# Performance work log

Measured on AMD Instinct MI355X. Metric: run time of the kernel, lower is better.

The kernel has to match this reference:

```python
import jax, jax.numpy as jnp
import numpy as np

H = 2048      # hidden_dim
NH = 32       # num_heads
HD = H // NH  # head_dim


def setup_inputs() -> dict:
    key = jax.random.key(0)
    ks = jax.random.split(key, 9)
    s = 1.0 / np.sqrt(H)
    return {
        "hidden_states": jax.random.normal(ks[0], (2, 2048, H), dtype=jnp.float32),
        "wq": jax.random.uniform(ks[1], (H, H), jnp.float32, -s, s),
        "bq": jnp.zeros((H,), jnp.float32),
        "wk": jax.random.uniform(ks[2], (H, H), jnp.float32, -s, s),
        "bk": jnp.zeros((H,), jnp.float32),
        "wv": jax.random.uniform(ks[3], (H, H), jnp.float32, -s, s),
        "bv": jnp.zeros((H,), jnp.float32),
        "wo": jax.random.uniform(ks[4], (H, H), jnp.float32, -s, s),
        "bo": jnp.zeros((H,), jnp.float32),
    }


def reference(hidden_states, wq, bq, wk, bk, wv, bv, wo, bo):
    B, S, _ = hidden_states.shape
    def heads(x):  # [B,S,H] -> [B,NH,S,HD]
        return x.reshape(B, S, NH, HD).transpose(0, 2, 1, 3)
    q = heads(hidden_states @ wq.T + bq)
    k = heads(hidden_states @ wk.T + bk)
    v = heads(hidden_states @ wv.T + bv)
    scores = jnp.einsum("bhqd,bhkd->bhqk", q, k) / np.sqrt(HD).astype(np.float32)
    causal = jnp.tril(jnp.ones((S, S), dtype=bool))
    scores = jnp.where(causal, scores, -jnp.inf)
    attn = jax.nn.softmax(scores, axis=-1)
    out = jnp.einsum("bhqk,bhkd->bhqd", attn, v)
    out = out.transpose(0, 2, 1, 3).reshape(B, S, H)
    return out @ wo.T + bo
```

## Files before the change

### kernel.cpp

```cpp
#include <hip/hip_runtime.h>
#include <hip/hip_bf16.h>

#define HDIM 2048
#define NHEADS 32
#define HEADD 64
#define NBATCH 2
#define SEQLEN 2048
#define MTOT (NBATCH * SEQLEN)
#define NQT (SEQLEN / 128)
#define LDQKV 6144

typedef __bf16 bf16;
typedef __bf16 bf16x8 __attribute__((ext_vector_type(8)));
typedef float f32x4 __attribute__((ext_vector_type(4)));
typedef float f32x8 __attribute__((ext_vector_type(8)));
typedef float f32x16 __attribute__((ext_vector_type(16)));

__device__ __forceinline__ void gload_lds16(const bf16* g, bf16* l) {
  __builtin_amdgcn_global_load_lds(
      (const __attribute__((address_space(1))) void*)g,
      (__attribute__((address_space(3))) void*)l, 16, 0, 0);
}

__device__ __forceinline__ unsigned cvtpk_bf16(float lo, float hi) {
  unsigned r;
  asm("v_cvt_pk_bf16_f32 %0, %1, %2" : "=v"(r) : "v"(lo), "v"(hi));
  return r;
}

__device__ __forceinline__ float max3f(float a, float b, float c) {
  float r;
  asm("v_max3_f32 %0, %1, %2, %3" : "=v"(r) : "v"(a), "v"(b), "v"(c));
  return r;
}

__global__ void __launch_bounds__(256) cvt_f32_to_bf16(
    const float* __restrict__ src, bf16* __restrict__ dst, int n) {
  int i = (blockIdx.x * 256 + threadIdx.x) * 8;
  if (i >= n) return;
  f32x8 a = *(const f32x8*)(src + i);
  bf16x8 o;
#pragma unroll
  for (int j = 0; j < 8; ++j) o[j] = (bf16)a[j];
  *(bf16x8*)(dst + i) = o;
}

__global__ void __launch_bounds__(256) cvt4_f32_to_bf16(
    const float* __restrict__ s0, const float* __restrict__ s1,
    const float* __restrict__ s2, const float* __restrict__ s3,
    bf16* __restrict__ d0, bf16* __restrict__ d1,
    bf16* __restrict__ d2, bf16* __restrict__ d3) {
  const float* src; bf16* dst;
  switch (blockIdx.y) {
    case 0: src = s0; dst = d0; break;
    case 1: src = s1; dst = d1; break;
    case 2: src = s2; dst = d2; break;
    default: src = s3; dst = d3; break;
  }
  int i = (blockIdx.x * 256 + threadIdx.x) * 8;
  f32x8 a = *(const f32x8*)(src + i);
  bf16x8 o;
#pragma unroll
  for (int j = 0; j < 8; ++j) o[j] = (bf16)a[j];
  *(bf16x8*)(dst + i) = o;
}

__global__ void __launch_bounds__(256) pack_bias(
    const float* __restrict__ bq, const float* __restrict__ bk,
    const float* __restrict__ bv, float* __restrict__ out) {
  int i = blockIdx.x * 256 + threadIdx.x;
  if (i >= LDQKV) return;
  float v;
  if (i < HDIM) v = bq[i];
  else if (i < 2 * HDIM) v = bk[i - HDIM];
  else v = bv[i - 2 * HDIM];
  out[i] = v;
}

template <bool OUT_F32>
__global__ void __launch_bounds__(256, 2) gemmq(
    const bf16* __restrict__ A, const bf16* __restrict__ W,
    const float* __restrict__ bias, void* __restrict__ Cout,
    int Ndim, float scale) {
  constexpr int NT = 64;
  __shared__ bf16 As[2][256 * 32];
  __shared__ bf16 Bs[3][192 * 32];

  const int tid = threadIdx.x;
  const int l = tid & 63;
  const int w = tid >> 6;
  const int wm = w >> 1;
  const int wn = w & 1;

  const int wid = blockIdx.x;
  const int j = wid >> 3;
  const int m0 = ((wid & 7) * 2 + (j & 1)) * 256;
  const int n0 = (j >> 1) * 192;

  const int rowA = tid >> 2;
  const int cg = (((tid & 3) ^ ((tid >> 3) & 3))) * 8;

  auto stgA = [&](int s, int kt) {
    const bf16* g = A + (size_t)m0 * 2048 + kt * 32 + cg;
#pragma unroll
    for (int i = 0; i < 4; ++i)
      gload_lds16(g + (size_t)(i * 64 + rowA) * 2048,
                  &As[s][(i * 256 + w * 64) * 8]);
  };
  auto stgB = [&](int s, int kt) {
    const bf16* g = W + (size_t)n0 * 2048 + kt * 32 + cg;
#pragma unroll
    for (int i = 0; i < 3; ++i)
      gload_lds16(g + (size_t)(i * 64 + rowA) * 2048,
                  &Bs[s][(i * 256 + w * 64) * 8]);
  };

  f32x4 acc[8][6];
#pragma unroll
  for (int mf = 0; mf < 8; ++mf)
#pragma unroll
    for (int nf = 0; nf < 6; ++nf) acc[mf][nf] = {0.f, 0.f, 0.f, 0.f};

  const int fr = l & 15;
  const int fch = (((l >> 4) ^ ((fr >> 1) & 3))) * 8;
  const int abase = (wm * 128 + fr) * 32 + fch;
  const int bbase = (wn * 96 + fr) * 32 + fch;

  stgA(0, 0);
  stgB(0, 0);
  stgB(1, 1);
  asm volatile("s_waitcnt vmcnt(3)" ::: "memory");
  __builtin_amdgcn_s_barrier();

  int sb = 0;
  for (int t = 0; t < NT; ++t) {
    const int sa = t & 1;
    int sb2 = sb + 2; if (sb2 >= 3) sb2 -= 3;

    bf16x8 bf[6], af[4];
#pragma unroll
    for (int nf = 0; nf < 6; ++nf)
      bf[nf] = *(const bf16x8*)&Bs[sb][bbase + nf * 16 * 32];
#pragma unroll
    for (int f = 0; f < 4; ++f)
      af[f] = *(const bf16x8*)&As[sa][abase + f * 16 * 32];

    if (t + 1 < NT) stgA(sa ^ 1, t + 1);
    if (t + 2 < NT) stgB(sb2, t + 2);

    __builtin_amdgcn_s_setprio(1);
#pragma unroll
    for (int f = 0; f < 4; ++f)
#pragma unroll
      for (int nf = 0; nf < 6; ++nf)
        acc[f][nf] = __builtin_amdgcn_mfma_f32_16x16x32_bf16(
            af[f], bf[nf], acc[f][nf], 0, 0, 0);
    __builtin_amdgcn_s_setprio(0);

#pragma unroll
    for (int f = 0; f < 4; ++f)
      af[f] = *(const bf16x8*)&As[sa][abase + (4 + f) * 16 * 32];

    __builtin_amdgcn_s_setprio(1);
#pragma unroll
    for (int f = 0; f < 4; ++f)
#pragma unroll
      for (int nf = 0; nf < 6; ++nf)
        acc[4 + f][nf] = __builtin_amdgcn_mfma_f32_16x16x32_bf16(
            af[f], bf[nf], acc[4 + f][nf], 0, 0, 0);
    __builtin_amdgcn_s_setprio(0);

    if (t < NT - 2)
      asm volatile("s_waitcnt vmcnt(3)" ::: "memory");
    else
      asm volatile("s_waitcnt vmcnt(0)" ::: "memory");
    __builtin_amdgcn_s_barrier();

    sb = (sb == 2) ? 0 : sb + 1;
  }

  const int rj = (l >> 4) * 4;
#pragma unroll
  for (int mf = 0; mf < 8; ++mf)
#pragma unroll
    for (int nf = 0; nf < 6; ++nf) {
      const int col = n0 + wn * 96 + nf * 16 + fr;
      const float secsc = (col < 2048) ? scale : 1.0f;
      const float bvl = bias[col];
#pragma unroll
      for (int jj = 0; jj < 4; ++jj) {
        const int row = m0 + wm * 128 + mf * 16 + rj + jj;
        const float v = (acc[mf][nf][jj] + bvl) * secsc;
        if constexpr (OUT_F32)
          ((float*)Cout)[(size_t)row * Ndim + col] = v;
        else
          ((bf16*)Cout)[(size_t)row * Ndim + col] = (bf16)v;
      }
    }
}

__global__ void __launch_bounds__(256, 2) gemmp(
    const bf16* __restrict__ A, const bf16* __restrict__ W,
    const float* __restrict__ bias, float* __restrict__ Cout,
    int Ndim) {
  constexpr int NT = 64;
  __shared__ bf16 As[2][128 * 32];
  __shared__ bf16 Bs[3][128 * 32];

  const int tid = threadIdx.x;
  const int l = tid & 63;
  const int w = tid >> 6;
  const int wm = w >> 1;
  const int wn = w & 1;

  const int wid = blockIdx.x;
  const int j = wid >> 3;
  const int m0 = ((wid & 7) * 4 + (j & 3)) * 128;
  const int n0 = (j >> 2) * 128;

  const int rowA = tid >> 2;
  const int cg = (((tid & 3) ^ ((tid >> 3) & 3))) * 8;

  auto stgA = [&](int s, int kt) {
    const bf16* g = A + (size_t)m0 * 2048 + kt * 32 + cg;
#pragma unroll
    for (int i = 0; i < 2; ++i)
      gload_lds16(g + (size_t)(i * 64 + rowA) * 2048,
                  &As[s][(i * 256 + w * 64) * 8]);
  };
  auto stgB = [&](int s, int kt) {
    const bf16* g = W + (size_t)n0 * 2048 + kt * 32 + cg;
#pragma unroll
    for (int i = 0; i < 2; ++i)
      gload_lds16(g + (size_t)(i * 64 + rowA) * 2048,
                  &Bs[s][(i * 256 + w * 64) * 8]);
  };

  f32x4 acc[4][4];
#pragma unroll
  for (int mf = 0; mf < 4; ++mf)
#pragma unroll
    for (int nf = 0; nf < 4; ++nf) acc[mf][nf] = {0.f, 0.f, 0.f, 0.f};

  const int fr = l & 15;
  const int fch = (((l >> 4) ^ ((fr >> 1) & 3))) * 8;
  const int abase = (wm * 64 + fr) * 32 + fch;
  const int bbase = (wn * 64 + fr) * 32 + fch;

  stgA(0, 0);
  stgB(0, 0);
  stgB(1, 1);
  asm volatile("s_waitcnt vmcnt(2)" ::: "memory");
  __builtin_amdgcn_s_barrier();

  int sb = 0;
  for (int t = 0; t < NT; ++t) {
    const int sa = t & 1;
    int sb2 = sb + 2; if (sb2 >= 3) sb2 -= 3;

    bf16x8 bf[4], af[4];
#pragma unroll
    for (int nf = 0; nf < 4; ++nf)
      bf[nf] = *(const bf16x8*)&Bs[sb][bbase + nf * 16 * 32];
#pragma unroll
    for (int f = 0; f < 4; ++f)
      af[f] = *(const bf16x8*)&As[sa][abase + f * 16 * 32];

    if (t + 1 < NT) stgA(sa ^ 1, t + 1);
    if (t + 2 < NT) stgB(sb2, t + 2);

    __builtin_amdgcn_s_setprio(1);
#pragma unroll
    for (int f = 0; f < 4; ++f)
#pragma unroll
      for (int nf = 0; nf < 4; ++nf)
        acc[f][nf] = __builtin_amdgcn_mfma_f32_16x16x32_bf16(
            af[f], bf[nf], acc[f][nf], 0, 0, 0);
    __builtin_amdgcn_s_setprio(0);

    if (t < NT - 2)
      asm volatile("s_waitcnt vmcnt(2)" ::: "memory");
    else
      asm volatile("s_waitcnt vmcnt(0)" ::: "memory");
    __builtin_amdgcn_s_barrier();

    sb = (sb == 2) ? 0 : sb + 1;
  }

  const int rj = (l >> 4) * 4;
#pragma unroll
  for (int mf = 0; mf < 4; ++mf)
#pragma unroll
    for (int nf = 0; nf < 4; ++nf) {
      const int col = n0 + wn * 64 + nf * 16 + fr;
      const float bvl = bias[col];
#pragma unroll
      for (int jj = 0; jj < 4; ++jj) {
        const int row = m0 + wm * 64 + mf * 16 + rj + jj;
        Cout[(size_t)row * Ndim + col] = acc[mf][nf][jj] + bvl;
      }
    }
}

__global__ void __launch_bounds__(256) transpose_v(
    const bf16* __restrict__ QKV, bf16* __restrict__ Vt) {
  __shared__ bf16 T[64][72];
  const int t = threadIdx.x;
  const int s0 = blockIdx.x * 64;
  const int h = blockIdx.y, b = blockIdx.z;
  const size_t inb = (size_t)b * SEQLEN * LDQKV + 2 * HDIM + (size_t)h * HEADD;
#pragma unroll
  for (int i = 0; i < 2; ++i) {
    const int idx = t + i * 256;
    const int r = idx >> 3, c = (idx & 7) * 8;
    *(bf16x8*)&T[r][c] = *(const bf16x8*)&QKV[inb + (size_t)(s0 + r) * LDQKV + c];
  }
  __syncthreads();
  const size_t outb = (size_t)(b * NHEADS + h) * HEADD * SEQLEN + s0;
#pragma unroll
  for (int i = 0; i < 2; ++i) {
    const int idx = t + i * 256;
    const int d = idx >> 3, cs = (idx & 7) * 8;
    bf16x8 o;
#pragma unroll
    for (int j = 0; j < 8; ++j) o[j] = T[cs + j][d];
    *(bf16x8*)&Vt[outb + (size_t)d * SEQLEN + cs] = o;
  }
}

__global__ void __launch_bounds__(256) attn4(
    const bf16* __restrict__ QKV, const bf16* __restrict__ Vt,
    bf16* __restrict__ O) {
  __shared__ bf16 Kl[2][64 * 64];
  __shared__ bf16 Vl[2][64 * 64];

  const int tid = threadIdx.x;
  const int l = tid & 63;
  const int w = tid >> 6;
  const int lq = l & 31;
  const int g = l >> 5;
  const int h = blockIdx.y, b = blockIdx.z;
  const size_t baseQ = (size_t)b * SEQLEN * LDQKV + (size_t)h * HEADD;
  const size_t baseK = baseQ + HDIM;
  const size_t baseV = (size_t)(b * NHEADS + h) * HEADD * SEQLEN;
  const size_t baseO = (size_t)b * SEQLEN * HDIM + (size_t)h * HEADD;

  const int L0 = w * 128 + l;
  const int L1 = w * 128 + 64 + l;
  const int r0 = L0 >> 3, gc0 = ((L0 & 7) ^ (r0 & 7)) * 8;
  const int r1 = L1 >> 3, gc1 = ((L1 & 7) ^ (r1 & 7)) * 8;
  const int dst0 = (w * 128) * 8;
  const int dst1 = (w * 128 + 64) * 8;

  auto stage = [&](int bufi, int kt) {
    const int k0s = kt * 64;
    gload_lds16(QKV + baseK + (size_t)(k0s + r0) * LDQKV + gc0, &Kl[bufi][dst0]);
    gload_lds16(QKV + baseK + (size_t)(k0s + r1) * LDQKV + gc1, &Kl[bufi][dst1]);
    gload_lds16(Vt + baseV + (size_t)r0 * SEQLEN + k0s + gc0, &Vl[bufi][dst0]);
    gload_lds16(Vt + baseV + (size_t)r1 * SEQLEN + k0s + gc1, &Vl[bufi][dst1]);
  };

#pragma unroll
  for (int seg = 0; seg < 2; ++seg) {
    const int qt = seg ? blockIdx.x : (NQT - 1 - blockIdx.x);
    const int q0 = qt * 128;
    const int qw = q0 + w * 32;
    const int qa = qw + lq;

    bf16x8 qf[4];
#pragma unroll
    for (int ks = 0; ks < 4; ++ks)
      qf[ks] = *(const bf16x8*)&QKV[baseQ + (size_t)qa * LDQKV + ks * 16 + g * 8];

    f32x16 oacc0, oacc1;
#pragma unroll
    for (int r = 0; r < 16; ++r) { oacc0[r] = 0.f; oacc1[r] = 0.f; }
    float mrun = -__builtin_inff(), lrun = 0.f;

    const int nkt = q0 / 64 + 2;
    stage(0, 0);

    for (int kt = 0; kt < nkt; ++kt) {
      const int cur = kt & 1;
      const int k0 = kt * 64;
      if (kt + 1 < nkt) {
        stage(cur ^ 1, kt + 1);
        asm volatile("s_waitcnt vmcnt(4)" ::: "memory");
      } else {
        asm volatile("s_waitcnt vmcnt(0)" ::: "memory");
      }
      __builtin_amdgcn_s_barrier();

      if (k0 <= qw + 31) {
        f32x16 st0, st1;
#pragma unroll
        for (int r = 0; r < 16; ++r) { st0[r] = 0.f; st1[r] = 0.f; }
        __builtin_amdgcn_s_setprio(1);
#pragma unroll
        for (int ks = 0; ks < 4; ++ks) {
          const int cr = (((2 * ks + g) ^ (lq & 7))) * 8;
          bf16x8 kf0 = *(const bf16x8*)&Kl[cur][lq * 64 + cr];
          bf16x8 kf1 = *(const bf16x8*)&Kl[cur][(32 + lq) * 64 + cr];
          st0 = __builtin_amdgcn_mfma_f32_32x32x16_bf16(kf0, qf[ks], st0, 0, 0, 0);
          st1 = __builtin_amdgcn_mfma_f32_32x32x16_bf16(kf1, qf[ks], st1, 0, 0, 0);
        }
        __builtin_amdgcn_s_setprio(0);

        if (k0 + 63 > qw) {
#pragma unroll
          for (int r = 0; r < 16; ++r) {
            const int ro = (r & 3) + 8 * (r >> 2) + 4 * g;
            if (k0 + ro > qa) st0[r] = -__builtin_inff();
            if (k0 + 32 + ro > qa) st1[r] = -__builtin_inff();
          }
        }

        float mx[8];
#pragma unroll
        for (int r = 0; r < 8; ++r)
          mx[r] = fmaxf(max3f(st0[r], st0[r + 8], st1[r]), st1[r + 8]);
        const float ma = max3f(mx[0], mx[1], mx[2]);
        const float mb = max3f(mx[3], mx[4], mx[5]);
        const float mc = max3f(mx[6], mx[7], ma);
        const float mtree = fmaxf(mb, mc);
        const float pm = fmaxf(mtree, __shfl_xor(mtree, 32));

        const float mnew = fmaxf(mrun, pm);
        if (!__all(pm - mrun <= 11.0f)) {
          const float sc = __builtin_amdgcn_exp2f(mrun - mnew);
          lrun *= sc;
#pragma unroll
          for (int r = 0; r < 16; ++r) {
            const int ro = (r & 3) + 8 * (r >> 2) + 4 * g;
            const float scr = __shfl(sc, ro);
            oacc0[r] *= scr;
            oacc1[r] *= scr;
          }
          mrun = mnew;
        }

#pragma unroll
        for (int r = 0; r < 16; ++r) {
          st0[r] = __builtin_amdgcn_exp2f(st0[r] - mrun);
          st1[r] = __builtin_amdgcn_exp2f(st1[r] - mrun);
        }
        float sm[8];
#pragma unroll
        for (int r = 0; r < 8; ++r)
          sm[r] = (st0[r] + st0[r + 8]) + (st1[r] + st1[r + 8]);
#pragma unroll
        for (int s = 4; s > 0; s >>= 1)
#pragma unroll
          for (int r = 0; r < 4; ++r)
            if (r < s) sm[r] += sm[r + s];
        lrun += sm[0] + __shfl_xor(sm[0], 32);

        unsigned wd0[8], wd1[8];
#pragma unroll
        for (int i = 0; i < 8; ++i) {
          wd0[i] = cvtpk_bf16(st0[2 * i], st0[2 * i + 1]);
          wd1[i] = cvtpk_bf16(st1[2 * i], st1[2 * i + 1]);
        }
        bf16x8 paf[4];
#pragma unroll
        for (int kt2 = 0; kt2 < 2; ++kt2)
#pragma unroll
          for (int hf = 0; hf < 2; ++hf) {
            const unsigned* wsrc = kt2 ? wd1 : wd0;
            const unsigned a0 = wsrc[hf * 4 + 0], a1 = wsrc[hf * 4 + 1];
            const unsigned b0 = wsrc[hf * 4 + 2], b1 = wsrc[hf * 4 + 3];
            const unsigned sb0 = (unsigned)__shfl_xor((int)b0, 32);
            const unsigned sb1 = (unsigned)__shfl_xor((int)b1, 32);
            const unsigned sa0 = (unsigned)__shfl_xor((int)a0, 32);
            const unsigned sa1 = (unsigned)__shfl_xor((int)a1, 32);
            union { unsigned u[4]; bf16x8 v; } fu;
            fu.u[0] = g ? sb0 : a0;
            fu.u[1] = g ? sb1 : a1;
            fu.u[2] = g ? b0 : sa0;
            fu.u[3] = g ? b1 : sa1;
            paf[kt2 * 2 + hf] = fu.v;
          }

        __builtin_amdgcn_s_setprio(1);
#pragma unroll
        for (int s = 0; s < 4; ++s) {
          const int cr = (((2 * s + g) ^ (lq & 7))) * 8;
          bf16x8 vf0 = *(const bf16x8*)&Vl[cur][lq * 64 + cr];
          bf16x8 vf1 = *(const bf16x8*)&Vl[cur][(32 + lq) * 64 + cr];
          oacc0 = __builtin_amdgcn_mfma_f32_32x32x16_bf16(paf[s], vf0, oacc0, 0, 0, 0);
          oacc1 = __builtin_amdgcn_mfma_f32_32x32x16_bf16(paf[s], vf1, oacc1, 0, 0, 0);
        }
        __builtin_amdgcn_s_setprio(0);
      }
      __builtin_amdgcn_s_barrier();
    }

#pragma unroll
    for (int r = 0; r < 16; ++r) {
      const int ro = (r & 3) + 8 * (r >> 2) + 4 * g;
      const float lr = __shfl(lrun, ro);
      const float inv = 1.0f / lr;
      O[baseO + (size_t)(qw + ro) * HDIM + lq] = (bf16)(oacc0[r] * inv);
      O[baseO + (size_t)(qw + ro) * HDIM + 32 + lq] = (bf16)(oacc1[r] * inv);
    }
  }
}

extern "C" void kernel_launch(void* const* d_in, const int* in_sizes, int n_in,
                              void* d_out, int out_size, void* d_ws, size_t ws_size,
                              hipStream_t stream) {
  (void)in_sizes; (void)n_in; (void)out_size; (void)ws_size;
  const float* hs = (const float*)d_in[0];
  const float* wq = (const float*)d_in[1];
  const float* bq = (const float*)d_in[2];
  const float* wk = (const float*)d_in[3];
  const float* bk = (const float*)d_in[4];
  const float* wv = (const float*)d_in[5];
  const float* bv = (const float*)d_in[6];
  const float* wo = (const float*)d_in[7];
  const float* bo = (const float*)d_in[8];

  char* wsp = (char*)d_ws;
  bf16* hsb  = (bf16*)wsp; wsp += (size_t)MTOT * HDIM * sizeof(bf16);
  bf16* wqb  = (bf16*)wsp; wsp += (size_t)HDIM * HDIM * sizeof(bf16);
  bf16* wkb  = (bf16*)wsp; wsp += (size_t)HDIM * HDIM * sizeof(bf16);
  bf16* wvb  = (bf16*)wsp; wsp += (size_t)HDIM * HDIM * sizeof(bf16);
  bf16* wob  = (bf16*)wsp; wsp += (size_t)HDIM * HDIM * sizeof(bf16);
  bf16* QKVb = (bf16*)wsp; wsp += (size_t)MTOT * LDQKV * sizeof(bf16);
  float* biasqkv = (float*)wsp; wsp += (size_t)LDQKV * sizeof(float);
  bf16* aob = hsb;
  bf16* Vtb = wqb;

  const int nHS = MTOT * HDIM;
  const int nW = HDIM * HDIM;
  cvt_f32_to_bf16<<<nHS / 2048, 256, 0, stream>>>(hs, hsb, nHS);
  dim3 gc(nW / 2048, 4);
  cvt4_f32_to_bf16<<<gc, 256, 0, stream>>>(wq, wk, wv, wo, wqb, wkb, wvb, wob);
  pack_bias<<<LDQKV / 256, 256, 0, stream>>>(bq, bk, bv, biasqkv);

  gemmq<false><<<dim3(512), 256, 0, stream>>>(
      hsb, wqb, biasqkv, QKVb, LDQKV, 0.125f * 1.44269504f);

  dim3 gt(SEQLEN / 64, NHEADS, NBATCH);
  transpose_v<<<gt, 256, 0, stream>>>(QKVb, Vtb);

  dim3 ga(NQT / 2, NHEADS, NBATCH);
  attn4<<<ga, 256, 0, stream>>>(QKVb, Vtb, aob);

  gemmp<<<dim3(512), 256, 0, stream>>>(aob, wob, bo, (float*)d_out, HDIM);
}
```

Before: 246.1 us.

## Software-pipeline QK^T of next tile with softmax/PV of current using triple-buffered LDS

Moves to a three-stage LDS ring for K and V and computes the QK^T MFMAs for tile t+1 before the softmax and PV work of tile t, so matrix ops can overlap the exp and reduction ALU work. The loop is unrolled by two so the score accumulators alternate between two register sets. It also replaces the shuffle-plus-select P-fragment exchange with v_permlane32_swap. The cost is more LDS per block and more live registers, which could lower occupancy. The unroll-by-two assumes nkt is even, which holds because q0 is a multiple of 128.

```diff
diff --git a/kernel.cpp b/kernel.cpp
--- a/kernel.cpp
+++ b/kernel.cpp
@@ -331,8 +331,8 @@
 __global__ void __launch_bounds__(256) attn4(
     const bf16* __restrict__ QKV, const bf16* __restrict__ Vt,
     bf16* __restrict__ O) {
-  __shared__ bf16 Kl[2][64 * 64];
-  __shared__ bf16 Vl[2][64 * 64];
+  __shared__ bf16 Kl[3][64 * 64];
+  __shared__ bf16 Vl[3][64 * 64];
 
   const int tid = threadIdx.x;
   const int l = tid & 63;
@@ -378,121 +378,133 @@
     float mrun = -__builtin_inff(), lrun = 0.f;
 
     const int nkt = q0 / 64 + 2;
+
+    auto qkt_f = [&](int buf, f32x16& s0, f32x16& s1) {
+#pragma unroll
+      for (int r = 0; r < 16; ++r) { s0[r] = 0.f; s1[r] = 0.f; }
+      __builtin_amdgcn_s_setprio(1);
+#pragma unroll
+      for (int ks = 0; ks < 4; ++ks) {
+        const int cr = (((2 * ks + g) ^ (lq & 7))) * 8;
+        bf16x8 kf0 = *(const bf16x8*)&Kl[buf][lq * 64 + cr];
+        bf16x8 kf1 = *(const bf16x8*)&Kl[buf][(32 + lq) * 64 + cr];
+        s0 = __builtin_amdgcn_mfma_f32_32x32x16_bf16(kf0, qf[ks], s0, 0, 0, 0);
+        s1 = __builtin_amdgcn_mfma_f32_32x32x16_bf16(kf1, qf[ks], s1, 0, 0, 0);
+      }
+      __builtin_amdgcn_s_setprio(0);
+    };
+
+    auto fin = [&](int t, f32x16& st0, f32x16& st1) {
+      const int k0 = t * 64;
+      if (k0 + 63 > qw) {
+#pragma unroll
+        for (int r = 0; r < 16; ++r) {
+          const int ro = (r & 3) + 8 * (r >> 2) + 4 * g;
+          if (k0 + ro > qa) st0[r] = -__builtin_inff();
+          if (k0 + 32 + ro > qa) st1[r] = -__builtin_inff();
+        }
+      }
+
+      float mx[8];
+#pragma unroll
+      for (int r = 0; r < 8; ++r)
+        mx[r] = fmaxf(max3f(st0[r], st0[r + 8], st1[r]), st1[r + 8]);
+      const float ma = max3f(mx[0], mx[1], mx[2]);
+      const float mb = max3f(mx[3], mx[4], mx[5]);
+      const float mc = max3f(mx[6], mx[7], ma);
+      const float mtree = fmaxf(mb, mc);
+      const float pm = fmaxf(mtree, __shfl_xor(mtree, 32));
+
+      const float mnew = fmaxf(mrun, pm);
+      if (!__all(pm - mrun <= 11.0f)) {
+        const float sc = __builtin_amdgcn_exp2f(mrun - mnew);
+        lrun *= sc;
+#pragma unroll
+        for (int r = 0; r < 16; ++r) {
+          const int ro = (r & 3) + 8 * (r >> 2) + 4 * g;
+          const float scr = __shfl(sc, ro);
+          oacc0[r] *= scr;
+          oacc1[r] *= scr;
+        }
+        mrun = mnew;
+      }
+
+#pragma unroll
+      for (int r = 0; r < 16; ++r) {
+        st0[r] = __builtin_amdgcn_exp2f(st0[r] - mrun);
+        st1[r] = __builtin_amdgcn_exp2f(st1[r] - mrun);
+      }
+      float sm[8];
+#pragma unroll
+      for (int r = 0; r < 8; ++r)
+        sm[r] = (st0[r] + st0[r + 8]) + (st1[r] + st1[r + 8]);
+#pragma unroll
+      for (int s = 4; s > 0; s >>= 1)
+#pragma unroll
+        for (int r = 0; r < 4; ++r)
+          if (r < s) sm[r] += sm[r + s];
+      lrun += sm[0] + __shfl_xor(sm[0], 32);
+
+      unsigned wd0[8], wd1[8];
+#pragma unroll
+      for (int i = 0; i < 8; ++i) {
+        wd0[i] = cvtpk_bf16(st0[2 * i], st0[2 * i + 1]);
+        wd1[i] = cvtpk_bf16(st1[2 * i], st1[2 * i + 1]);
+      }
+      bf16x8 paf[4];
+#pragma unroll
+      for (int kt2 = 0; kt2 < 2; ++kt2)
+#pragma unroll
+        for (int hf = 0; hf < 2; ++hf) {
+          unsigned* wsrc = kt2 ? wd1 : wd0;
+          unsigned pa = wsrc[hf * 4 + 0], pb = wsrc[hf * 4 + 1];
+          unsigned qa2 = wsrc[hf * 4 + 2], qb2 = wsrc[hf * 4 + 3];
+          asm("v_permlane32_swap_b32 %0, %1" : "+v"(pa), "+v"(qa2));
+          asm("v_permlane32_swap_b32 %0, %1" : "+v"(pb), "+v"(qb2));
+          union { unsigned u[4]; bf16x8 v; } fu;
+          fu.u[0] = pa; fu.u[1] = pb; fu.u[2] = qa2; fu.u[3] = qb2;
+          paf[kt2 * 2 + hf] = fu.v;
+        }
+
+      const int bc = t % 3;
+      __builtin_amdgcn_s_setprio(1);
+#pragma unroll
+      for (int s = 0; s < 4; ++s) {
+        const int cr = (((2 * s + g) ^ (lq & 7))) * 8;
+        bf16x8 vf0 = *(const bf16x8*)&Vl[bc][lq * 64 + cr];
+        bf16x8 vf1 = *(const bf16x8*)&Vl[bc][(32 + lq) * 64 + cr];
+        oacc0 = __builtin_amdgcn_mfma_f32_32x32x16_bf16(paf[s], vf0, oacc0, 0, 0, 0);
+        oacc1 = __builtin_amdgcn_mfma_f32_32x32x16_bf16(paf[s], vf1, oacc1, 0, 0, 0);
+      }
+      __builtin_amdgcn_s_setprio(0);
+    };
+
+    f32x16 sA0, sA1, sB0, sB1;
+
     stage(0, 0);
-
-    for (int kt = 0; kt < nkt; ++kt) {
-      const int cur = kt & 1;
-      const int k0 = kt * 64;
-      if (kt + 1 < nkt) {
-        stage(cur ^ 1, kt + 1);
+    stage(1, 1);
+    asm volatile("s_waitcnt vmcnt(4)" ::: "memory");
+    __builtin_amdgcn_s_barrier();
+    qkt_f(0, sA0, sA1);
+
+    auto body = [&](int t, f32x16& c0, f32x16& c1, f32x16& n0, f32x16& n1) {
+      if (t + 2 < nkt) {
+        stage((t + 2) % 3, t + 2);
         asm volatile("s_waitcnt vmcnt(4)" ::: "memory");
       } else {
         asm volatile("s_waitcnt vmcnt(0)" ::: "memory");
       }
       __builtin_amdgcn_s_barrier();
-
-      if (k0 <= qw + 31) {
-        f32x16 st0, st1;
-#pragma unroll
-        for (int r = 0; r < 16; ++r) { st0[r] = 0.f; st1[r] = 0.f; }
-        __builtin_amdgcn_s_setprio(1);
-#pragma unroll
-        for (int ks = 0; ks < 4; ++ks) {
-          const int cr = (((2 * ks + g) ^ (lq & 7))) * 8;
-          bf16x8 kf0 = *(const bf16x8*)&Kl[cur][lq * 64 + cr];
-          bf16x8 kf1 = *(const bf16x8*)&Kl[cur][(32 + lq) * 64 + cr];
-          st0 = __builtin_amdgcn_mfma_f32_32x32x16_bf16(kf0, qf[ks], st0, 0, 0, 0);
-          st1 = __builtin_amdgcn_mfma_f32_32x32x16_bf16(kf1, qf[ks], st1, 0, 0, 0);
-        }
-        __builtin_amdgcn_s_setprio(0);
-
-        if (k0 + 63 > qw) {
-#pragma unroll
-          for (int r = 0; r < 16; ++r) {
-            const int ro = (r & 3) + 8 * (r >> 2) + 4 * g;
-            if (k0 + ro > qa) st0[r] = -__builtin_inff();
-            if (k0 + 32 + ro > qa) st1[r] = -__builtin_inff();
-          }
-        }
-
-        float mx[8];
-#pragma unroll
-        for (int r = 0; r < 8; ++r)
-          mx[r] = fmaxf(max3f(st0[r], st0[r + 8], st1[r]), st1[r + 8]);
-        const float ma = max3f(mx[0], mx[1], mx[2]);
-        const float mb = max3f(mx[3], mx[4], mx[5]);
-        const float mc = max3f(mx[6], mx[7], ma);
-        const float mtree = fmaxf(mb, mc);
-        const float pm = fmaxf(mtree, __shfl_xor(mtree, 32));
-
-        const float mnew = fmaxf(mrun, pm);
-        if (!__all(pm - mrun <= 11.0f)) {
-          const float sc = __builtin_amdgcn_exp2f(mrun - mnew);
-          lrun *= sc;
-#pragma unroll
-          for (int r = 0; r < 16; ++r) {
-            const int ro = (r & 3) + 8 * (r >> 2) + 4 * g;
-            const float scr = __shfl(sc, ro);
-            oacc0[r] *= scr;
-            oacc1[r] *= scr;
-          }
-          mrun = mnew;
-        }
-
-#pragma unroll
-        for (int r = 0; r < 16; ++r) {
-          st0[r] = __builtin_amdgcn_exp2f(st0[r] - mrun);
-          st1[r] = __builtin_amdgcn_exp2f(st1[r] - mrun);
-        }
-        float sm[8];
-#pragma unroll
-        for (int r = 0; r < 8; ++r)
-          sm[r] = (st0[r] + st0[r + 8]) + (st1[r] + st1[r + 8]);
-#pragma unroll
-        for (int s = 4; s > 0; s >>= 1)
-#pragma unroll
-          for (int r = 0; r < 4; ++r)
-            if (r < s) sm[r] += sm[r + s];
-        lrun += sm[0] + __shfl_xor(sm[0], 32);
-
-        unsigned wd0[8], wd1[8];
-#pragma unroll
-        for (int i = 0; i < 8; ++i) {
-          wd0[i] = cvtpk_bf16(st0[2 * i], st0[2 * i + 1]);
-          wd1[i] = cvtpk_bf16(st1[2 * i], st1[2 * i + 1]);
-        }
-        bf16x8 paf[4];
-#pragma unroll
-        for (int kt2 = 0; kt2 < 2; ++kt2)
-#pragma unroll
-          for (int hf = 0; hf < 2; ++hf) {
-            const unsigned* wsrc = kt2 ? wd1 : wd0;
-            const unsigned a0 = wsrc[hf * 4 + 0], a1 = wsrc[hf * 4 + 1];
-            const unsigned b0 = wsrc[hf * 4 + 2], b1 = wsrc[hf * 4 + 3];
-            const unsigned sb0 = (unsigned)__shfl_xor((int)b0, 32);
-            const unsigned sb1 = (unsigned)__shfl_xor((int)b1, 32);
-            const unsigned sa0 = (unsigned)__shfl_xor((int)a0, 32);
-            const unsigned sa1 = (unsigned)__shfl_xor((int)a1, 32);
-            union { unsigned u[4]; bf16x8 v; } fu;
-            fu.u[0] = g ? sb0 : a0;
-            fu.u[1] = g ? sb1 : a1;
-            fu.u[2] = g ? b0 : sa0;
-            fu.u[3] = g ? b1 : sa1;
-            paf[kt2 * 2 + hf] = fu.v;
-          }
-
-        __builtin_amdgcn_s_setprio(1);
-#pragma unroll
-        for (int s = 0; s < 4; ++s) {
-          const int cr = (((2 * s + g) ^ (lq & 7))) * 8;
-          bf16x8 vf0 = *(const bf16x8*)&Vl[cur][lq * 64 + cr];
-          bf16x8 vf1 = *(const bf16x8*)&Vl[cur][(32 + lq) * 64 + cr];
-          oacc0 = __builtin_amdgcn_mfma_f32_32x32x16_bf16(paf[s], vf0, oacc0, 0, 0, 0);
-          oacc1 = __builtin_amdgcn_mfma_f32_32x32x16_bf16(paf[s], vf1, oacc1, 0, 0, 0);
-        }
-        __builtin_amdgcn_s_setprio(0);
-      }
+      if (t + 1 < nkt && (t + 1) * 64 <= qw + 31)
+        qkt_f((t + 1) % 3, n0, n1);
+      if (t * 64 <= qw + 31)
+        fin(t, c0, c1);
       __builtin_amdgcn_s_barrier();
+    };
+
+    for (int t = 0; t < nkt; t += 2) {
+      body(t, sA0, sA1, sB0, sB1);
+      body(t + 1, sB0, sB1, sA0, sA1);
     }
 
 #pragma unroll
```

Result: slower. 287.7 us (+16.9%).
